# Kernel tuning notes

Measured on AMD Instinct MI355X. Metric: run time of the kernel, lower is better.

## Reference

```python
import jax, jax.numpy as jnp
import numpy as np

B, N, C, NH = 4, 4096, 192, 3
H = W = 64
HD = C // NH  # 64
K_SPA = [8, 4, 2]
SCALE = C ** (-0.5)
LN_EPS = 1e-5


def _ln(x, g, b):
    m = jnp.mean(x, axis=-1, keepdims=True)
    v = jnp.mean(jnp.square(x - m), axis=-1, keepdims=True)
    return (x - m) * jax.lax.rsqrt(v + LN_EPS) * g + b


def _conv2d(x, w, b, padding='VALID', groups=1):
    y = jax.lax.conv_general_dilated(
        x, w, window_strides=(1, 1), padding=padding,
        dimension_numbers=('NCHW', 'OIHW', 'NCHW'), feature_group_count=groups)
    return y + b[None, :, None, None]


def _branch(x_img, q_h, kv_w, kv_b, sr_w, sr_b, ln_g, ln_b, lc_w, lc_b):
    # x_img: [B,C,H,W]; q_h: [B,N,HD]
    f = _conv2d(x_img, sr_w, sr_b)                      # [B,C,h',w'] (VALID, stride 1)
    m = f.shape[2] * f.shape[3]
    side = f.shape[2]                                   # square: h'==w'
    t = f.reshape(B, C, m).transpose(0, 2, 1)           # [B,m,C]
    t = jax.nn.gelu(_ln(t, ln_g, ln_b), approximate=False)
    kv = (t @ kv_w.T + kv_b).reshape(B, m, NH, HD)      # head-split of kv proj
    k = kv[:, :, 0, :]                                  # [B,m,HD] (head 0 -> k)
    v = kv[:, :, 1, :]                                  # [B,m,HD] (head 1 -> v)
    attn = jax.nn.softmax(jnp.einsum('bnd,bmd->bnm', q_h, k) * SCALE, axis=-1)
    v_img = v.transpose(0, 2, 1).reshape(B, HD, side, side)
    v = v + _conv2d(v_img, lc_w, lc_b, padding=((1, 1), (1, 1)), groups=HD)\
        .reshape(B, HD, m).transpose(0, 2, 1)           # local depthwise conv added to V
    return jnp.einsum('bnm,bmd->bnd', attn, v)          # [B,N,HD]


def _fwd(x, q_w, q_b, kv_w, kv_b, sr1_w, sr1_b, sr2_w, sr2_b, sr3_w, sr3_b,
         ln1_g, ln1_b, ln2_g, ln2_b, ln3_g, ln3_b,
         lc1_w, lc1_b, lc2_w, lc2_b, lc3_w, lc3_b, nn1_w, nn1_b):
    q = (x @ q_w.T + q_b).reshape(B, N, NH, HD).transpose(0, 2, 1, 3)  # [B,NH,N,HD]
    x_img = x.transpose(0, 2, 1).reshape(B, C, H, W)
    x1 = _branch(x_img, q[:, 0], kv_w, kv_b, sr1_w, sr1_b, ln1_g, ln1_b, lc1_w, lc1_b)
    x2 = _branch(x_img, q[:, 1], kv_w, kv_b, sr2_w, sr2_b, ln2_g, ln2_b, lc2_w, lc2_b)
    x3 = _branch(x_img, q[:, 2], kv_w, kv_b, sr3_w, sr3_b, ln3_g, ln3_b, lc3_w, lc3_b)
    out = jnp.concatenate([x1, x2, x3], axis=-1)        # [B,N,C]
    return out @ nn1_w.T + nn1_b


def setup_inputs() -> dict:
    key = jax.random.key(0)
    ks = jax.random.split(key, 16)
    s = lambda i, shp: (jax.random.normal(ks[i], shp, jnp.float32) * 0.02)
    d = dict(
        x=jax.random.normal(ks[0], (B, N, C), jnp.float32),
        q_w=s(1, (C, C)), q_b=jnp.zeros((C,), jnp.float32),
        kv_w=s(2, (C, C)), kv_b=jnp.zeros((C,), jnp.float32),
        sr1_w=s(3, (C, C, K_SPA[0], K_SPA[0])), sr1_b=jnp.zeros((C,), jnp.float32),
        sr2_w=s(4, (C, C, K_SPA[1], K_SPA[1])), sr2_b=jnp.zeros((C,), jnp.float32),
        sr3_w=s(5, (C, C, K_SPA[2], K_SPA[2])), sr3_b=jnp.zeros((C,), jnp.float32),
        ln1_g=jnp.ones((C,), jnp.float32), ln1_b=jnp.zeros((C,), jnp.float32),
        ln2_g=jnp.ones((C,), jnp.float32), ln2_b=jnp.zeros((C,), jnp.float32),
        ln3_g=jnp.ones((C,), jnp.float32), ln3_b=jnp.zeros((C,), jnp.float32),
        lc1_w=s(6, (HD, 1, 3, 3)), lc1_b=jnp.zeros((HD,), jnp.float32),
        lc2_w=s(7, (HD, 1, 3, 3)), lc2_b=jnp.zeros((HD,), jnp.float32),
        lc3_w=s(8, (HD, 1, 3, 3)), lc3_b=jnp.zeros((HD,), jnp.float32),
        nn1_w=s(9, (C, C)), nn1_b=jnp.zeros((C,), jnp.float32),
    )
    return d


def reference(x, q_w, q_b, kv_w, kv_b, sr1_w, sr1_b, sr2_w, sr2_b, sr3_w, sr3_b,
              ln1_g, ln1_b, ln2_g, ln2_b, ln3_g, ln3_b,
              lc1_w, lc1_b, lc2_w, lc2_b, lc3_w, lc3_b, nn1_w, nn1_b):
    return _fwd(x, q_w, q_b, kv_w, kv_b, sr1_w, sr1_b, sr2_w, sr2_b, sr3_w, sr3_b,
                ln1_g, ln1_b, ln2_g, ln2_b, ln3_g, ln3_b,
                lc1_w, lc1_b, lc2_w, lc2_b, lc3_w, lc3_b, nn1_w, nn1_b)
```

## Files before the change

### kernel.cpp

```cpp
#include <hip/hip_runtime.h>
#include <hip/hip_bf16.h>

typedef unsigned short u16;
typedef unsigned int   u32;
typedef __attribute__((ext_vector_type(8))) short bf16x8;
typedef __attribute__((ext_vector_type(4))) float f32x4;

#define DI static __device__ __forceinline__
#define MFMA(a,b,c) __builtin_amdgcn_mfma_f32_16x16x32_bf16(a,b,c,0,0,0)

static constexpr int CB = 192;
static constexpr int NB = 4096;
static constexpr int BB = 4;
static constexpr float SCALE = 0.07216878364870323f;

DI float b2f(u16 u){ union{u32 i; float f;} x; x.i = (u32)u << 16; return x.f; }
DI u16 f2b(float f){ union{u32 i; float f;} x; x.f = f;
  u32 r = x.i + 0x7FFFu + ((x.i >> 16) & 1u); return (u16)(r >> 16); }

DI int swzb(int row, int byteInRow){ return row*128 + (byteInRow ^ ((row & 7) << 4)); }

template<bool F32>
DI void stage16(const void* base, size_t eoff, char* dst, int srow, int q4){
  if (F32){
    const float* s = (const float*)base + eoff;
    float4 a0 = *(const float4*)(s);
    float4 a1 = *(const float4*)(s + 4);
    float4 a2 = *(const float4*)(s + 8);
    float4 a3 = *(const float4*)(s + 12);
    union { uint4 v; u16 h[8]; } r0, r1;
    r0.h[0]=f2b(a0.x); r0.h[1]=f2b(a0.y); r0.h[2]=f2b(a0.z); r0.h[3]=f2b(a0.w);
    r0.h[4]=f2b(a1.x); r0.h[5]=f2b(a1.y); r0.h[6]=f2b(a1.z); r0.h[7]=f2b(a1.w);
    r1.h[0]=f2b(a2.x); r1.h[1]=f2b(a2.y); r1.h[2]=f2b(a2.z); r1.h[3]=f2b(a2.w);
    r1.h[4]=f2b(a3.x); r1.h[5]=f2b(a3.y); r1.h[6]=f2b(a3.z); r1.h[7]=f2b(a3.w);
    *(uint4*)(dst + swzb(srow, q4*32))      = r0.v;
    *(uint4*)(dst + swzb(srow, q4*32 + 16)) = r1.v;
  } else {
    const u16* s = (const u16*)base + eoff;
    *(uint4*)(dst + swzb(srow, q4*32))      = *(const uint4*)(s);
    *(uint4*)(dst + swzb(srow, q4*32 + 16)) = *(const uint4*)(s + 8);
  }
}

__global__ __launch_bounds__(256) void cvt_k(const float* __restrict__ in,
      u16* __restrict__ out, int n4){
  int i = blockIdx.x*256 + threadIdx.x;
  if (i >= n4) return;
  float4 v = ((const float4*)in)[i];
  union{ uint2 u; u16 h[4]; } r;
  r.h[0]=f2b(v.x); r.h[1]=f2b(v.y); r.h[2]=f2b(v.z); r.h[3]=f2b(v.w);
  ((uint2*)out)[i] = r.u;
}

template<int K>
__global__ void repack_k(const float* __restrict__ w, u16* __restrict__ wt, int total){
  int i = blockIdx.x*256 + threadIdx.x;
  if (i >= total) return;
  int kk  = i / (CB*CB);
  int rem = i % (CB*CB);
  int co = rem / CB, ci = rem % CB;
  int ky = kk / K, kx = kk % K;
  wt[i] = f2b(w[((co*CB + ci)*K + ky)*K + kx]);
}

template<int K>
__global__ __launch_bounds__(512) void conv_k(const u16* __restrict__ xb,
      const u16* __restrict__ wt, const float* __restrict__ bias,
      u16* __restrict__ out, int side, int m){
  constexpr int AR = K*64;
  __shared__ char lds[(AR + 2*192)*128];
  char* Awin = lds;
  char* W0 = lds + AR*128;
  char* W1 = W0 + 192*128;

  const int t = threadIdx.x;
  const int l = t & 63, lr = l & 15, lg = l >> 4;
  const int ww = (t >> 6) & 3, wg = t >> 8;
  const int b = blockIdx.x / side;
  const int oy = blockIdx.x % side;

  int boff[6][2];
  #pragma unroll
  for (int f = 0; f < 6; ++f){
    boff[f][0] = swzb(96*wg + 16*f + lr, lg*16);
    boff[f][1] = swzb(96*wg + 16*f + lr, 64 + lg*16);
  }

  f32x4 zero = {0.f,0.f,0.f,0.f};
  f32x4 acc[6];
  #pragma unroll
  for (int f = 0; f < 6; ++f) acc[f] = zero;

  const int rowb = 16*ww + lr;

  for (int c0 = 0; c0 < CB; c0 += 64){
    __syncthreads();
    #pragma unroll
    for (int k = 0; k < (K*256 + 511)/512; ++k){
      int s = t + k*512;
      if (s < K*256){
        int row = s >> 2, q4 = s & 3;
        int r = row >> 6, scol = row & 63;
        stage16<false>(xb, ((size_t)(b*NB + (oy + r)*64 + scol))*CB + c0 + q4*16,
                       Awin, row, q4);
      }
    }
    #pragma unroll
    for (int k = 0; k < 2; ++k){
      int s = t + k*512;
      if (s < 768){
        int row = s >> 2, q4 = s & 3;
        stage16<false>(wt, ((size_t)row)*CB + c0 + q4*16, W0, row, q4);
      }
    }
    for (int kk = 0; kk < K*K; ++kk){
      __syncthreads();
      char* Wcur = (kk & 1) ? W1 : W0;
      if (kk + 1 < K*K){
        char* Wnxt = (kk & 1) ? W0 : W1;
        #pragma unroll
        for (int k = 0; k < 2; ++k){
          int s = t + k*512;
          if (s < 768){
            int row = s >> 2, q4 = s & 3;
            stage16<false>(wt, ((size_t)(kk+1)*CB + row)*CB + c0 + q4*16, Wnxt, row, q4);
          }
        }
      }
      int ky = kk / K, kx = kk - ky*K;
      int arow = ky*64 + rowb + kx;
      int x16 = (arow & 7) << 4;
      const char* ab = Awin + arow*128;
      bf16x8 a0 = *(const bf16x8*)(ab + ((lg*16) ^ x16));
      bf16x8 a1 = *(const bf16x8*)(ab + ((64 + lg*16) ^ x16));
      #pragma unroll
      for (int f = 0; f < 6; ++f){
        bf16x8 b0v = *(const bf16x8*)(Wcur + boff[f][0]);
        bf16x8 b1v = *(const bf16x8*)(Wcur + boff[f][1]);
        acc[f] = MFMA(a0, b0v, acc[f]);
        acc[f] = MFMA(a1, b1v, acc[f]);
      }
    }
  }

  const int posb = oy*side;
  #pragma unroll
  for (int f = 0; f < 6; ++f){
    int co = 96*wg + 16*f + lr;
    float bv = bias[co];
    #pragma unroll
    for (int r = 0; r < 4; ++r){
      int ox = 16*ww + lg*4 + r;
      if (ox < side)
        out[((size_t)(b*m + posb + ox))*CB + co] = f2b(acc[f][r] + bv);
    }
  }
}

struct GemmP {
  const void* A; const void* W; const float* bias;
  u16* outb; u16* outk; u16* outv; float* outf;
  int Mtot;
  int m;
  int mtiles, ntiles;
};

template<int EPI, bool AF32, bool WF32>
__global__ __launch_bounds__(256) void gemm_k(GemmP p){
  __shared__ uint4 ldsbuf[1024];
  char* ldsA = (char*)ldsbuf;
  char* ldsB = ldsA + 8192;

  const int t = threadIdx.x;
  const int w = t >> 6, l = t & 63, lr = l & 15, lg = l >> 4;

  int bid = blockIdx.x;
  int nt = bid % p.ntiles, mt = bid / p.ntiles;

  const int srow = t >> 2;
  const int q4   = t & 3;

  size_t abase;
  { int row = mt*64 + srow; if (row > p.Mtot - 1) row = p.Mtot - 1;
    abase = (size_t)row * CB; }
  const int wrow = nt*64 + srow;

  const int aoff0 = swzb(16*w + lr, lg*16);
  const int aoff1 = swzb(16*w + lr, 64 + lg*16);
  int boff[4][2];
  #pragma unroll
  for (int f = 0; f < 4; ++f){ boff[f][0] = swzb(16*f + lr, lg*16); boff[f][1] = swzb(16*f + lr, 64 + lg*16); }

  f32x4 zero = {0.f,0.f,0.f,0.f};
  f32x4 acc[4] = {zero, zero, zero, zero};

  size_t wbase = (size_t)wrow * CB;
  for (int c0 = 0; c0 < CB; c0 += 64){
    stage16<AF32>(p.A, abase + c0 + q4*16, ldsA, srow, q4);
    stage16<WF32>(p.W, wbase + c0 + q4*16, ldsB, srow, q4);
    __syncthreads();
    bf16x8 a0 = *(const bf16x8*)(ldsA + aoff0);
    bf16x8 a1 = *(const bf16x8*)(ldsA + aoff1);
    #pragma unroll
    for (int f = 0; f < 4; ++f){
      bf16x8 b0 = *(const bf16x8*)(ldsB + boff[f][0]);
      bf16x8 b1 = *(const bf16x8*)(ldsB + boff[f][1]);
      acc[f] = MFMA(a0, b0, acc[f]);
      acc[f] = MFMA(a1, b1, acc[f]);
    }
    __syncthreads();
  }

  #pragma unroll
  for (int f = 0; f < 4; ++f){
    #pragma unroll
    for (int r = 0; r < 4; ++r){
      int rowt = 16*w + lg*4 + r;
      int col  = nt*64 + 16*f + lr;
      float v = acc[f][r] + p.bias[col];
      int grow = mt*64 + rowt;
      if (grow >= p.Mtot) continue;
      if (EPI == 0){
        p.outb[(size_t)grow*CB + col] = f2b(v);
      } else if (EPI == 2){
        int bb = grow / p.m, pp = grow % p.m;
        if (col < 64) p.outk[(size_t)(bb*p.m + pp)*64 + col]        = f2b(v);
        else          p.outv[(size_t)(bb*p.m + pp)*64 + (col - 64)] = f2b(v);
      } else {
        p.outf[(size_t)grow*CB + col] = v;
      }
    }
  }
}

__global__ __launch_bounds__(256) void ln_gelu_k(const u16* __restrict__ tp,
      const float* __restrict__ g, const float* __restrict__ bt,
      u16* __restrict__ out, int rows){
  int w = threadIdx.x >> 6, l = threadIdx.x & 63;
  int p = blockIdx.x*4 + w;
  if (p >= rows) return;
  const u16* rp = tp + (size_t)p*CB;
  float x0 = b2f(rp[l]), x1 = b2f(rp[l+64]), x2 = b2f(rp[l+128]);
  float s = x0 + x1 + x2;
  #pragma unroll
  for (int d = 1; d < 64; d <<= 1) s += __shfl_xor(s, d);
  float mean = s * (1.0f/192.0f);
  float d0 = x0-mean, d1 = x1-mean, d2 = x2-mean;
  float q = d0*d0 + d1*d1 + d2*d2;
  #pragma unroll
  for (int d = 1; d < 64; d <<= 1) q += __shfl_xor(q, d);
  float rstd = rsqrtf(q * (1.0f/192.0f) + 1e-5f);
  u16* op = out + (size_t)p*CB;
  float dv[3] = {d0, d1, d2};
  #pragma unroll
  for (int i = 0; i < 3; ++i){
    int c = l + i*64;
    float xv = dv[i] * rstd * g[c] + bt[c];
    float ge = 0.5f * xv * (1.0f + erff(xv * 0.7071067811865475f));
    op[c] = f2b(ge);
  }
}

__global__ __launch_bounds__(256) void lcconv_k(const u16* __restrict__ vpre,
      const float* __restrict__ lw, const float* __restrict__ lb,
      u16* __restrict__ vt, int m, int mpad, int side){
  int w = threadIdx.x >> 6, d = threadIdx.x & 63;
  int idx = blockIdx.x*4 + w;
  if (idx >= BB*m) return;
  int b = idx / m, p = idx % m;
  int h = p / side, x = p % side;
  float acc = b2f(vpre[(size_t)idx*64 + d]);
  float wv[9];
  #pragma unroll
  for (int j = 0; j < 9; ++j) wv[j] = lw[d*9 + j];
  #pragma unroll
  for (int dy = 0; dy < 3; ++dy){
    int hh = h + dy - 1;
    if (hh < 0 || hh >= side) continue;
    #pragma unroll
    for (int dx = 0; dx < 3; ++dx){
      int ww = x + dx - 1;
      if (ww < 0 || ww >= side) continue;
      acc += b2f(vpre[(size_t)(b*m + hh*side + ww)*64 + d]) * wv[dy*3 + dx];
    }
  }
  acc += lb[d];
  vt[(size_t)(b*64 + d)*mpad + p] = f2b(acc);
}

__global__ __launch_bounds__(512) void attn_k(const u16* __restrict__ qall,
      const u16* __restrict__ kbuf, const u16* __restrict__ vt,
      u16* __restrict__ xh, int m, int mpad, int head){
  __shared__ char lds[57344];
  char* Qb = lds;
  char* Kb = lds + 8192;
  char* Vb = lds + 24576;
  char* Pb = lds + 40960;
  const int t = threadIdx.x;
  const int w = t >> 6, l = t & 63, lr = l & 15, lg = l >> 4;
  const int ww = w & 3, wg = w >> 2;
  char* Kg = Kb + wg*8192;
  char* Vg = Vb + wg*8192;
  char* Pw = Pb + w*2048;
  const int b = blockIdx.x >> 6, q0 = (blockIdx.x & 63)*64;

  if (t < 256){
    int row = t >> 2, seg = (t & 3)*32;
    const char* src = (const char*)(qall + (size_t)(b*NB + q0 + row)*CB + head*64) + seg;
    *(uint4*)(Qb + swzb(row, seg))    = *(const uint4*)src;
    *(uint4*)(Qb + swzb(row, seg+16)) = *(const uint4*)(src + 16);
  }

  const int qoff0 = swzb(16*ww + lr, lg*16), qoff1 = swzb(16*ww + lr, 64 + lg*16);
  int koff[4][2];
  #pragma unroll
  for (int f = 0; f < 4; ++f){ koff[f][0] = swzb(16*f + lr, lg*16); koff[f][1] = swzb(16*f + lr, 64 + lg*16); }
  const int poff0 = swzb(lr, lg*16), poff1 = swzb(lr, 64 + lg*16);

  float mrow[4] = {-1e30f,-1e30f,-1e30f,-1e30f};
  float lrow[4] = {0.f,0.f,0.f,0.f};
  f32x4 zero = {0.f,0.f,0.f,0.f};
  f32x4 oacc[4] = {zero, zero, zero, zero};

  const int nkc = (m + 63) / 64;
  const int cmax = (nkc + 1) >> 1;
  const int tt = t & 255;
  for (int it = 0; it < cmax; ++it){
    const int kc = it*2 + wg;
    const bool active = kc < nkc;
    const int j0 = kc*64;
    __syncthreads();
    if (active){
      int j = tt >> 2, seg = (tt & 3)*32;
      int jj = j0 + j; if (jj > m-1) jj = m-1;
      const char* src = (const char*)(kbuf + (size_t)(b*m + jj)*64) + seg;
      *(uint4*)(Kg + swzb(j, seg))    = *(const uint4*)src;
      *(uint4*)(Kg + swzb(j, seg+16)) = *(const uint4*)(src + 16);
      int d = j;
      const char* sv = (const char*)(vt + (size_t)(b*64 + d)*mpad + j0) + seg;
      *(uint4*)(Vg + swzb(d, seg))    = *(const uint4*)sv;
      *(uint4*)(Vg + swzb(d, seg+16)) = *(const uint4*)(sv + 16);
    }
    __syncthreads();
    if (active){
      f32x4 s[4] = {zero, zero, zero, zero};
      bf16x8 a0 = *(const bf16x8*)(Qb + qoff0);
      bf16x8 a1 = *(const bf16x8*)(Qb + qoff1);
      #pragma unroll
      for (int f = 0; f < 4; ++f){
        bf16x8 k0 = *(const bf16x8*)(Kg + koff[f][0]);
        bf16x8 k1 = *(const bf16x8*)(Kg + koff[f][1]);
        s[f] = MFMA(a0, k0, s[f]);
        s[f] = MFMA(a1, k1, s[f]);
      }
      float fac[4];
      #pragma unroll
      for (int r = 0; r < 4; ++r){
        float mx = -1e30f;
        #pragma unroll
        for (int f = 0; f < 4; ++f){
          float sv = s[f][r] * SCALE;
          int key = j0 + 16*f + lr;
          sv = (key < m) ? sv : -1e30f;
          s[f][r] = sv;
          mx = fmaxf(mx, sv);
        }
        mx = fmaxf(mx, __shfl_xor(mx, 1));
        mx = fmaxf(mx, __shfl_xor(mx, 2));
        mx = fmaxf(mx, __shfl_xor(mx, 4));
        mx = fmaxf(mx, __shfl_xor(mx, 8));
        float mold = mrow[r];
        float mnew = fmaxf(mold, mx);
        mrow[r] = mnew;
        fac[r] = __expf(mold - mnew);
        float rs = 0.f;
        #pragma unroll
        for (int f = 0; f < 4; ++f){
          float pe = __expf(s[f][r] - mnew);
          rs += pe;
          int prow = lg*4 + r, pcol = 16*f + lr;
          *(u16*)(Pw + swzb(prow, pcol*2)) = f2b(pe);
        }
        rs += __shfl_xor(rs, 1);
        rs += __shfl_xor(rs, 2);
        rs += __shfl_xor(rs, 4);
        rs += __shfl_xor(rs, 8);
        lrow[r] = lrow[r]*fac[r] + rs;
      }
      #pragma unroll
      for (int f = 0; f < 4; ++f){
        oacc[f][0] *= fac[0]; oacc[f][1] *= fac[1];
        oacc[f][2] *= fac[2]; oacc[f][3] *= fac[3];
      }
    }
    __syncthreads();
    if (active){
      bf16x8 p0 = *(const bf16x8*)(Pw + poff0);
      bf16x8 p1 = *(const bf16x8*)(Pw + poff1);
      #pragma unroll
      for (int f = 0; f < 4; ++f){
        bf16x8 v0 = *(const bf16x8*)(Vg + koff[f][0]);
        bf16x8 v1 = *(const bf16x8*)(Vg + koff[f][1]);
        oacc[f] = MFMA(p0, v0, oacc[f]);
        oacc[f] = MFMA(p1, v1, oacc[f]);
      }
    }
  }

  __syncthreads();
  if (wg == 1){
    char* Mb = Kb + ww*6144;
    #pragma unroll
    for (int f = 0; f < 4; ++f) *(f32x4*)(Mb + l*64 + f*16) = oacc[f];
    float4 mm = {mrow[0], mrow[1], mrow[2], mrow[3]};
    *(float4*)(Mb + 4096 + l*16) = mm;
    float4 ll = {lrow[0], lrow[1], lrow[2], lrow[3]};
    *(float4*)(Mb + 5120 + l*16) = ll;
  }
  __syncthreads();
  if (wg == 0){
    char* Mb = Kb + ww*6144;
    float4 m1 = *(const float4*)(Mb + 4096 + l*16);
    float4 l1 = *(const float4*)(Mb + 5120 + l*16);
    float M1[4] = {m1.x, m1.y, m1.z, m1.w};
    float L1[4] = {l1.x, l1.y, l1.z, l1.w};
    #pragma unroll
    for (int r = 0; r < 4; ++r){
      float M = fmaxf(mrow[r], M1[r]);
      float e0 = __expf(mrow[r] - M), e1 = __expf(M1[r] - M);
      float lt = lrow[r]*e0 + L1[r]*e1;
      #pragma unroll
      for (int f = 0; f < 4; ++f){
        float o1 = ((const f32x4*)(Mb + l*64 + f*16))[0][r];
        float val = (oacc[f][r]*e0 + o1*e1) / lt;
        int row = q0 + 16*ww + lg*4 + r;
        int col = head*64 + 16*f + lr;
        xh[(size_t)(b*NB + row)*CB + col] = f2b(val);
      }
    }
  }
}

extern "C" void kernel_launch(void* const* d_in, const int* in_sizes, int n_in,
                              void* d_out, int out_size, void* d_ws, size_t ws_size,
                              hipStream_t stream){
  const float* x     = (const float*)d_in[0];
  const float* q_w   = (const float*)d_in[1];
  const float* q_b   = (const float*)d_in[2];
  const float* kv_w  = (const float*)d_in[3];
  const float* kv_b  = (const float*)d_in[4];
  const float* sr_w[3] = {(const float*)d_in[5], (const float*)d_in[7], (const float*)d_in[9]};
  const float* sr_b[3] = {(const float*)d_in[6], (const float*)d_in[8], (const float*)d_in[10]};
  const float* ln_g[3] = {(const float*)d_in[11], (const float*)d_in[13], (const float*)d_in[15]};
  const float* ln_b[3] = {(const float*)d_in[12], (const float*)d_in[14], (const float*)d_in[16]};
  const float* lc_w[3] = {(const float*)d_in[17], (const float*)d_in[19], (const float*)d_in[21]};
  const float* lc_b[3] = {(const float*)d_in[18], (const float*)d_in[20], (const float*)d_in[22]};
  const float* nn1_w = (const float*)d_in[23];
  const float* nn1_b = (const float*)d_in[24];

  char* ws = (char*)d_ws;
  u16* q_all  = (u16*)d_out;
  u16* xb     = (u16*)(ws);
  u16* xheads = (u16*)(ws + 6291456);
  u16* wt     = (u16*)(ws + 12582912);
  u16* kbuf   = (u16*)(ws + 12582912);
  u16* vpre   = (u16*)(ws + 14615040);
  u16* tpre   = (u16*)(ws + 17301504);
  u16* vtb    = (u16*)(ws + 17301504);
  u16* tbuf   = (u16*)(ws + 23397888);

  const int Ks[3] = {8, 4, 2}, sides[3] = {57, 61, 63};

  cvt_k<<<3072, 256, 0, stream>>>(x, xb, 786432);

  {
    GemmP p{}; p.A = xb; p.W = q_w; p.bias = q_b; p.outb = q_all;
    p.Mtot = BB*NB; p.m = BB*NB; p.mtiles = 256; p.ntiles = 3;
    gemm_k<0,false,true><<<256*3, 256, 0, stream>>>(p);
  }

  for (int i = 0; i < 3; ++i){
    const int K = Ks[i], side = sides[i], m = side*side;
    const int mpad = ((m + 64 + 7)/8)*8;
    const int tot = CB*CB*K*K;
    if (i == 0) repack_k<8><<<(tot+255)/256, 256, 0, stream>>>(sr_w[i], wt, tot);
    if (i == 1) repack_k<4><<<(tot+255)/256, 256, 0, stream>>>(sr_w[i], wt, tot);
    if (i == 2) repack_k<2><<<(tot+255)/256, 256, 0, stream>>>(sr_w[i], wt, tot);

    if (i == 0) conv_k<8><<<BB*side, 512, 0, stream>>>(xb, wt, sr_b[i], tpre, side, m);
    if (i == 1) conv_k<4><<<BB*side, 512, 0, stream>>>(xb, wt, sr_b[i], tpre, side, m);
    if (i == 2) conv_k<2><<<BB*side, 512, 0, stream>>>(xb, wt, sr_b[i], tpre, side, m);

    ln_gelu_k<<<m, 256, 0, stream>>>(tpre, ln_g[i], ln_b[i], tbuf, BB*m);

    GemmP pk{}; pk.A = tbuf; pk.W = kv_w; pk.bias = kv_b; pk.outk = kbuf; pk.outv = vpre;
    pk.Mtot = BB*m; pk.m = m; pk.mtiles = (BB*m + 63)/64; pk.ntiles = 2;
    gemm_k<2,false,true><<<pk.mtiles*2, 256, 0, stream>>>(pk);

    lcconv_k<<<m, 256, 0, stream>>>(vpre, lc_w[i], lc_b[i], vtb, m, mpad, side);

    attn_k<<<BB*64, 512, 0, stream>>>(q_all, kbuf, vtb, xheads, m, mpad, i);
  }

  {
    GemmP p{}; p.A = xheads; p.W = nn1_w; p.bias = nn1_b; p.outf = (float*)d_out;
    p.Mtot = BB*NB; p.m = BB*NB; p.mtiles = 256; p.ntiles = 3;
    gemm_k<3,false,true><<<256*3, 256, 0, stream>>>(p);
  }
}
```

Measured before the change: 702.3 us.

## Split conv output channels across blocks and double-buffer input rows and weights

The spatial-reduction conv kernel now uses 256-thread blocks, each computing half of the output channels, which doubles the grid. Input rows are staged one kernel row at a time into double-buffered LDS alongside double-buffered weight tiles, and each block's weight fragments are reused across two A row tiles. The weight repack kernel is also rewritten so each thread reads one contiguous K*K filter and writes strided outputs. The aim is smaller LDS use, higher occupancy and more parallelism, at the cost of loading each input window twice, once per channel half.

```diff
diff --git a/kernel.cpp b/kernel.cpp
--- a/kernel.cpp
+++ b/kernel.cpp
@@ -53,106 +53,118 @@
 }
 
 template<int K>
-__global__ void repack_k(const float* __restrict__ w, u16* __restrict__ wt, int total){
-  int i = blockIdx.x*256 + threadIdx.x;
-  if (i >= total) return;
-  int kk  = i / (CB*CB);
-  int rem = i % (CB*CB);
-  int co = rem / CB, ci = rem % CB;
-  int ky = kk / K, kx = kk % K;
-  wt[i] = f2b(w[((co*CB + ci)*K + ky)*K + kx]);
+__global__ __launch_bounds__(256) void repack_k(const float* __restrict__ w,
+      u16* __restrict__ wt){
+  int rem = blockIdx.x*256 + threadIdx.x;
+  if (rem >= CB*CB) return;
+  const float* src = w + (size_t)rem*K*K;
+  #pragma unroll
+  for (int kk = 0; kk < K*K; ++kk)
+    wt[(size_t)kk*CB*CB + rem] = f2b(src[kk]);
 }
 
 template<int K>
-__global__ __launch_bounds__(512) void conv_k(const u16* __restrict__ xb,
+__global__ __launch_bounds__(256) void conv_k(const u16* __restrict__ xb,
       const u16* __restrict__ wt, const float* __restrict__ bias,
       u16* __restrict__ out, int side, int m){
-  constexpr int AR = K*64;
-  __shared__ char lds[(AR + 2*192)*128];
-  char* Awin = lds;
-  char* W0 = lds + AR*128;
-  char* W1 = W0 + 192*128;
+  __shared__ char lds[43008];
+  char* Ab0 = lds;
+  char* Ab1 = lds + 9216;
+  char* Wb0 = lds + 18432;
+  char* Wb1 = lds + 30720;
 
   const int t = threadIdx.x;
   const int l = t & 63, lr = l & 15, lg = l >> 4;
-  const int ww = (t >> 6) & 3, wg = t >> 8;
-  const int b = blockIdx.x / side;
-  const int oy = blockIdx.x % side;
-
-  int boff[6][2];
-  #pragma unroll
-  for (int f = 0; f < 6; ++f){
-    boff[f][0] = swzb(96*wg + 16*f + lr, lg*16);
-    boff[f][1] = swzb(96*wg + 16*f + lr, 64 + lg*16);
+  const int w = t >> 6;
+  const int wa = w & 1, wbh = w >> 1;
+
+  int bid = blockIdx.x;
+  const int nh = bid & 1; bid >>= 1;
+  const int b = bid / side;
+  const int oy = bid % side;
+
+  int boff[3][2];
+  #pragma unroll
+  for (int f = 0; f < 3; ++f){
+    int row = wbh*48 + f*16 + lr;
+    boff[f][0] = swzb(row, lg*16);
+    boff[f][1] = swzb(row, 64 + lg*16);
   }
 
   f32x4 zero = {0.f,0.f,0.f,0.f};
-  f32x4 acc[6];
-  #pragma unroll
-  for (int f = 0; f < 6; ++f) acc[f] = zero;
-
-  const int rowb = 16*ww + lr;
-
-  for (int c0 = 0; c0 < CB; c0 += 64){
+  f32x4 acc[2][3];
+  #pragma unroll
+  for (int fa = 0; fa < 2; ++fa)
+    #pragma unroll
+    for (int fb = 0; fb < 3; ++fb) acc[fa][fb] = zero;
+
+  const int sr = t >> 2, sq = t & 3;
+
+  auto STAGEW = [&](int kkg, int c0, char* dst){
+    stage16<false>(wt, ((size_t)kkg*CB + nh*96 + sr)*CB + c0 + sq*16, dst, sr, sq);
+    if (t < 128){
+      int r2 = sr + 64;
+      stage16<false>(wt, ((size_t)kkg*CB + nh*96 + r2)*CB + c0 + sq*16, dst, r2, sq);
+    }
+  };
+  auto STAGEA = [&](int ky, int c0, char* dst){
+    int cc = sr > 63 ? 63 : sr;
+    stage16<false>(xb, ((size_t)(b*NB + (oy+ky)*64 + cc))*CB + c0 + sq*16, dst, sr, sq);
+    if (t < 32){
+      int r2 = sr + 64;
+      stage16<false>(xb, ((size_t)(b*NB + (oy+ky)*64 + 63))*CB + c0 + sq*16, dst, r2, sq);
+    }
+  };
+
+  STAGEA(0, 0, Ab0);
+  STAGEW(0, 0, Wb0);
+  const int NPH = 3*K*K;
+  for (int g = 0; g < NPH; ++g){
     __syncthreads();
-    #pragma unroll
-    for (int k = 0; k < (K*256 + 511)/512; ++k){
-      int s = t + k*512;
-      if (s < K*256){
-        int row = s >> 2, q4 = s & 3;
-        int r = row >> 6, scol = row & 63;
-        stage16<false>(xb, ((size_t)(b*NB + (oy + r)*64 + scol))*CB + c0 + q4*16,
-                       Awin, row, q4);
-      }
-    }
-    #pragma unroll
-    for (int k = 0; k < 2; ++k){
-      int s = t + k*512;
-      if (s < 768){
-        int row = s >> 2, q4 = s & 3;
-        stage16<false>(wt, ((size_t)row)*CB + c0 + q4*16, W0, row, q4);
-      }
-    }
-    for (int kk = 0; kk < K*K; ++kk){
-      __syncthreads();
-      char* Wcur = (kk & 1) ? W1 : W0;
-      if (kk + 1 < K*K){
-        char* Wnxt = (kk & 1) ? W0 : W1;
-        #pragma unroll
-        for (int k = 0; k < 2; ++k){
-          int s = t + k*512;
-          if (s < 768){
-            int row = s >> 2, q4 = s & 3;
-            stage16<false>(wt, ((size_t)(kk+1)*CB + row)*CB + c0 + q4*16, Wnxt, row, q4);
-          }
-        }
-      }
-      int ky = kk / K, kx = kk - ky*K;
-      int arow = ky*64 + rowb + kx;
-      int x16 = (arow & 7) << 4;
-      const char* ab = Awin + arow*128;
+    int c0i = g/(K*K); int rem = g - c0i*K*K; int kx = rem % K;
+    int gn = g + 1;
+    if (gn < NPH){
+      int c0n = gn/(K*K); int remn = gn - c0n*K*K;
+      STAGEW(remn, c0n*64, (gn & 1) ? Wb1 : Wb0);
+      if ((remn % K) == 0)
+        STAGEA(remn / K, c0n*64, ((gn/K) & 1) ? Ab1 : Ab0);
+    }
+    char* Wc = (g & 1) ? Wb1 : Wb0;
+    bf16x8 wf[3][2];
+    #pragma unroll
+    for (int f = 0; f < 3; ++f){
+      wf[f][0] = *(const bf16x8*)(Wc + boff[f][0]);
+      wf[f][1] = *(const bf16x8*)(Wc + boff[f][1]);
+    }
+    char* Ac = ((g/K) & 1) ? Ab1 : Ab0;
+    #pragma unroll
+    for (int fa = 0; fa < 2; ++fa){
+      int c = wa*32 + fa*16 + lr + kx;
+      int x16 = (c & 7) << 4;
+      const char* ab = Ac + c*128;
       bf16x8 a0 = *(const bf16x8*)(ab + ((lg*16) ^ x16));
       bf16x8 a1 = *(const bf16x8*)(ab + ((64 + lg*16) ^ x16));
       #pragma unroll
-      for (int f = 0; f < 6; ++f){
-        bf16x8 b0v = *(const bf16x8*)(Wcur + boff[f][0]);
-        bf16x8 b1v = *(const bf16x8*)(Wcur + boff[f][1]);
-        acc[f] = MFMA(a0, b0v, acc[f]);
-        acc[f] = MFMA(a1, b1v, acc[f]);
+      for (int fb = 0; fb < 3; ++fb){
+        acc[fa][fb] = MFMA(a0, wf[fb][0], acc[fa][fb]);
+        acc[fa][fb] = MFMA(a1, wf[fb][1], acc[fa][fb]);
       }
     }
   }
 
   const int posb = oy*side;
   #pragma unroll
-  for (int f = 0; f < 6; ++f){
-    int co = 96*wg + 16*f + lr;
+  for (int fb = 0; fb < 3; ++fb){
+    int co = nh*96 + wbh*48 + fb*16 + lr;
     float bv = bias[co];
     #pragma unroll
-    for (int r = 0; r < 4; ++r){
-      int ox = 16*ww + lg*4 + r;
-      if (ox < side)
-        out[((size_t)(b*m + posb + ox))*CB + co] = f2b(acc[f][r] + bv);
+    for (int fa = 0; fa < 2; ++fa){
+      #pragma unroll
+      for (int r = 0; r < 4; ++r){
+        int ox = wa*32 + fa*16 + lg*4 + r;
+        if (ox < side)
+          out[((size_t)(b*m + posb + ox))*CB + co] = f2b(acc[fa][fb][r] + bv);
+      }
     }
   }
 }
@@ -482,14 +494,13 @@
   for (int i = 0; i < 3; ++i){
     const int K = Ks[i], side = sides[i], m = side*side;
     const int mpad = ((m + 64 + 7)/8)*8;
-    const int tot = CB*CB*K*K;
-    if (i == 0) repack_k<8><<<(tot+255)/256, 256, 0, stream>>>(sr_w[i], wt, tot);
-    if (i == 1) repack_k<4><<<(tot+255)/256, 256, 0, stream>>>(sr_w[i], wt, tot);
-    if (i == 2) repack_k<2><<<(tot+255)/256, 256, 0, stream>>>(sr_w[i], wt, tot);
-
-    if (i == 0) conv_k<8><<<BB*side, 512, 0, stream>>>(xb, wt, sr_b[i], tpre, side, m);
-    if (i == 1) conv_k<4><<<BB*side, 512, 0, stream>>>(xb, wt, sr_b[i], tpre, side, m);
-    if (i == 2) conv_k<2><<<BB*side, 512, 0, stream>>>(xb, wt, sr_b[i], tpre, side, m);
+    if (i == 0) repack_k<8><<<144, 256, 0, stream>>>(sr_w[i], wt);
+    if (i == 1) repack_k<4><<<144, 256, 0, stream>>>(sr_w[i], wt);
+    if (i == 2) repack_k<2><<<144, 256, 0, stream>>>(sr_w[i], wt);
+
+    if (i == 0) conv_k<8><<<BB*side*2, 256, 0, stream>>>(xb, wt, sr_b[i], tpre, side, m);
+    if (i == 1) conv_k<4><<<BB*side*2, 256, 0, stream>>>(xb, wt, sr_b[i], tpre, side, m);
+    if (i == 2) conv_k<2><<<BB*side*2, 256, 0, stream>>>(xb, wt, sr_b[i], tpre, side, m);
 
     ln_gelu_k<<<m, 256, 0, stream>>>(tpre, ln_g[i], ln_b[i], tbuf, BB*m);
 
```

Result: faster. 682.5 us (-2.8%).
